# Kernel optimization log

Hardware: AMD Instinct MI355X
Metric: run time of the kernel (lower is better)

Reference implementation:

```python
import jax, jax.numpy as jnp
import numpy as np

D_MODEL = 256; N_HEADS = 8; N_LEVELS = 4; N_POINTS = 4; D_FFN = 1024
SHAPES = [(128, 128), (64, 64), (32, 32), (16, 16)]  # (H, W) per level, strides 8/16/32/64 of 1024x1024 input
B = 8; LQ = 1024
S_TOT = sum(h * w for h, w in SHAPES)


def setup_inputs() -> dict:
    key = jax.random.key(0)
    ks = iter(jax.random.split(key, 48))
    d = D_MODEL

    def f(shape, s=0.02):
        return jax.random.normal(next(ks), shape, dtype=jnp.float32) * s

    return {
        'tgt': f((B, LQ, d), 1.0),
        'query_pos': f((B, LQ, d), 1.0),
        'reference_points': jax.random.uniform(next(ks), (B, LQ, N_LEVELS, 2), dtype=jnp.float32),
        'src': f((B, S_TOT, d), 1.0),
        'w_in': f((3 * d, d)), 'b_in': jnp.zeros((3 * d,), jnp.float32),
        'w_out': f((d, d)), 'b_out': jnp.zeros((d,), jnp.float32),
        'ln1_g': jnp.ones((d,), jnp.float32), 'ln1_b': jnp.zeros((d,), jnp.float32),
        'ln2_g': jnp.ones((d,), jnp.float32), 'ln2_b': jnp.zeros((d,), jnp.float32),
        'ln3_g': jnp.ones((d,), jnp.float32), 'ln3_b': jnp.zeros((d,), jnp.float32),
        'w_val': f((d, d)), 'b_val': jnp.zeros((d,), jnp.float32),
        'w_off': f((N_HEADS * N_LEVELS * N_POINTS * 2, d), 0.002),
        'b_off': f((N_HEADS * N_LEVELS * N_POINTS * 2,), 0.5),
        'w_attw': f((N_HEADS * N_LEVELS * N_POINTS, d)),
        'b_attw': jnp.zeros((N_HEADS * N_LEVELS * N_POINTS,), jnp.float32),
        'w_oc': f((d, d)), 'b_oc': jnp.zeros((d,), jnp.float32),
        'w1': f((D_FFN, d)), 'b1': jnp.zeros((D_FFN,), jnp.float32),
        'w2': f((d, D_FFN)), 'b2': jnp.zeros((d,), jnp.float32),
        'spatial_shapes': jnp.array(SHAPES, dtype=jnp.int32),
    }


def layer_norm(x, g, b):
    mu = x.mean(-1, keepdims=True)
    var = ((x - mu) ** 2).mean(-1, keepdims=True)
    return (x - mu) * jax.lax.rsqrt(var + 1e-5) * g + b


def mha(tgt, query_pos, w_in, b_in, w_out, b_out):
    d = D_MODEL; Dh = d // N_HEADS
    Bs, Lq, _ = tgt.shape
    qk = tgt + query_pos
    q = (qk @ w_in[:d].T + b_in[:d]).reshape(Bs, Lq, N_HEADS, Dh)
    k = (qk @ w_in[d:2 * d].T + b_in[d:2 * d]).reshape(Bs, Lq, N_HEADS, Dh)
    v = (tgt @ w_in[2 * d:].T + b_in[2 * d:]).reshape(Bs, Lq, N_HEADS, Dh)
    attn = jax.nn.softmax(jnp.einsum('bqhd,bkhd->bhqk', q, k) / np.sqrt(Dh).astype(np.float32), axis=-1)
    o = jnp.einsum('bhqk,bkhd->bqhd', attn, v).reshape(Bs, Lq, d)
    return o @ w_out.T + b_out


def ms_deform_attn(value, loc, attw):
    # value [B,S,H,Dh]; loc [B,Lq,H,L,P,2] in [0,1]; attw [B,Lq,H,L,P]
    Bs, _, Hh, Dh = value.shape
    Lq = loc.shape[1]

    def to_hfirst(x):  # [B,Lq,Hh,P] -> [B,Hh,Lq*P,1]
        return jnp.transpose(x, (0, 2, 1, 3)).reshape(Bs, Hh, Lq * N_POINTS, 1)

    acc = jnp.zeros((Bs, Hh, Lq * N_POINTS, Dh), value.dtype)
    start = 0
    for l, (H_, W_) in enumerate(SHAPES):
        v = jnp.transpose(value[:, start:start + H_ * W_], (0, 2, 1, 3))  # [B,Hh,HW,Dh]
        start += H_ * W_
        ll = loc[:, :, :, l]  # [B,Lq,Hh,P,2]
        x = ll[..., 0] * W_ - 0.5
        y = ll[..., 1] * H_ - 0.5
        x0 = jnp.floor(x); y0 = jnp.floor(y)
        tx = x - x0; ty = y - y0

        def gather(xi, yi):
            valid = ((xi >= 0) & (xi < W_) & (yi >= 0) & (yi < H_)).astype(value.dtype)
            fi = (jnp.clip(yi, 0, H_ - 1) * W_ + jnp.clip(xi, 0, W_ - 1)).astype(jnp.int32)
            g = jnp.take_along_axis(v, to_hfirst(fi.astype(jnp.float32)).astype(jnp.int32), axis=2)
            return g * to_hfirst(valid)

        samp = (gather(x0, y0) * to_hfirst((1 - tx) * (1 - ty))
                + gather(x0 + 1, y0) * to_hfirst(tx * (1 - ty))
                + gather(x0, y0 + 1) * to_hfirst((1 - tx) * ty)
                + gather(x0 + 1, y0 + 1) * to_hfirst(tx * ty))
        acc = acc + samp * to_hfirst(attw[:, :, :, l])
    out = acc.reshape(Bs, Hh, Lq, N_POINTS, Dh).sum(3)  # [B,Hh,Lq,Dh]
    return jnp.transpose(out, (0, 2, 1, 3)).reshape(Bs, Lq, Hh * Dh)


def reference(tgt, query_pos, reference_points, src, w_in, b_in, w_out, b_out,
              ln1_g, ln1_b, ln2_g, ln2_b, ln3_g, ln3_b,
              w_val, b_val, w_off, b_off, w_attw, b_attw, w_oc, b_oc,
              w1, b1, w2, b2, spatial_shapes):
    Bs, Lq, d = tgt.shape
    Dh = d // N_HEADS
    # --- self attention (q=k=tgt+pos, v=tgt), residual + norm2 ---
    t2 = mha(tgt, query_pos, w_in, b_in, w_out, b_out)
    tgt = layer_norm(tgt + t2, ln2_g, ln2_b)
    # --- MSDeformAttn cross attention, residual + norm1 ---
    query = tgt + query_pos
    value = (src @ w_val.T + b_val).reshape(Bs, -1, N_HEADS, Dh)
    off = (query @ w_off.T + b_off).reshape(Bs, Lq, N_HEADS, N_LEVELS, N_POINTS, 2)
    aw = jax.nn.softmax((query @ w_attw.T + b_attw).reshape(Bs, Lq, N_HEADS, N_LEVELS * N_POINTS), axis=-1)
    aw = aw.reshape(Bs, Lq, N_HEADS, N_LEVELS, N_POINTS)
    normalizer = jnp.array([[w, h] for h, w in SHAPES], dtype=tgt.dtype)  # (W,H) per level
    loc = reference_points[:, :, None, :, None, :] + off / normalizer[None, None, None, :, None, :]
    ca = ms_deform_attn(value, loc, aw) @ w_oc.T + b_oc
    tgt = layer_norm(tgt + ca, ln1_g, ln1_b)
    # --- FFN, residual + norm3 ---
    t2 = jax.nn.relu(tgt @ w1.T + b1) @ w2.T + b2
    tgt = layer_norm(tgt + t2, ln3_g, ln3_b)
    return tgt
```

## Files before the change

kernel.cpp:

```cpp
#include <hip/hip_runtime.h>

typedef unsigned short ushort_t;
typedef unsigned int uint_t;
typedef __attribute__((ext_vector_type(8))) short short8;
typedef __attribute__((ext_vector_type(4))) float floatx4;
typedef __attribute__((ext_vector_type(4))) unsigned short ushortx4;

__device__ __forceinline__ ushort_t f2bf(float f){
  uint_t u = __builtin_bit_cast(uint_t, f);
  u += 0x7FFFu + ((u >> 16) & 1u);
  return (ushort_t)(u >> 16);
}
__device__ __forceinline__ float bf2f(ushort_t u){
  uint_t x = ((uint_t)u) << 16;
  return __builtin_bit_cast(float, x);
}
__device__ __forceinline__ uint_t packbf2(float a, float b){
  return (uint_t)f2bf(a) | ((uint_t)f2bf(b) << 16);
}

__device__ __forceinline__ void gload16(const void* g, void* l){
  __builtin_amdgcn_global_load_lds(
      (const __attribute__((address_space(1))) void*)g,
      (__attribute__((address_space(3))) void*)l, 16, 0, 0);
}

#define FENCED_BARRIER() asm volatile("s_barrier" ::: "memory")

__global__ __launch_bounds__(256) void convert_w_kernel(const float* __restrict__ w_in,
    const float* __restrict__ w_val, const float* __restrict__ w_out,
    const float* __restrict__ w_oc, const float* __restrict__ w1,
    const float* __restrict__ w2, const float* __restrict__ w_off,
    const float* __restrict__ w_attw, ushort_t* __restrict__ dst){
  int j = (blockIdx.x*256 + threadIdx.x) * 4;
  if (j >= 1015808) return;
  const float* src; int off;
  if      (j < 196608){ src = w_in;   off = 0;      }
  else if (j < 262144){ src = w_val;  off = 196608; }
  else if (j < 327680){ src = w_out;  off = 262144; }
  else if (j < 393216){ src = w_oc;   off = 327680; }
  else if (j < 655360){ src = w1;     off = 393216; }
  else if (j < 917504){ src = w2;     off = 655360; }
  else if (j < 983040){ src = w_off;  off = 917504; }
  else                { src = w_attw; off = 983040; }
  float4 v = *(const float4*)(src + (j - off));
  uint2 u; u.x = packbf2(v.x, v.y); u.y = packbf2(v.z, v.w);
  *(uint2*)(dst + j) = u;
}

__global__ __launch_bounds__(256) void pack_bias_kernel(const float* __restrict__ b_off,
    const float* __restrict__ b_attw, float* __restrict__ dst){
  int t = threadIdx.x;
  dst[t] = b_off[t];
  if (t < 128) dst[256 + t] = b_attw[t];
}

__global__ __launch_bounds__(256) void add_kernel(const float* __restrict__ a,
    const float* __restrict__ b, float* __restrict__ c, int n4){
  int i = blockIdx.x * 256 + threadIdx.x;
  if (i < n4){
    float4 x = ((const float4*)a)[i];
    float4 y = ((const float4*)b)[i];
    float4 z; z.x=x.x+y.x; z.y=x.y+y.y; z.z=x.z+y.z; z.w=x.w+y.w;
    ((float4*)c)[i] = z;
  }
}

__global__ __launch_bounds__(256) void addln_kernel(const float* __restrict__ X,
    const float* __restrict__ Y, const float* __restrict__ gw,
    const float* __restrict__ bw, float* __restrict__ Out){
  int wave = threadIdx.x >> 6, lane = threadIdx.x & 63;
  long row = (long)blockIdx.x * 4 + wave;
  long base = row * 256 + lane * 4;
  float4 x = *(const float4*)(X + base);
  float4 y = *(const float4*)(Y + base);
  float v0=x.x+y.x, v1=x.y+y.y, v2=x.z+y.z, v3=x.w+y.w;
  float s  = v0+v1+v2+v3;
  float sq = v0*v0+v1*v1+v2*v2+v3*v3;
  #pragma unroll
  for (int off=32; off>0; off>>=1){
    s  += __shfl_xor(s, off);
    sq += __shfl_xor(sq, off);
  }
  float mu  = s * (1.f/256.f);
  float var = sq * (1.f/256.f) - mu*mu;
  float rs  = rsqrtf(var + 1e-5f);
  float4 g4 = *(const float4*)(gw + lane*4);
  float4 b4 = *(const float4*)(bw + lane*4);
  float4 o;
  o.x = (v0-mu)*rs*g4.x + b4.x;
  o.y = (v1-mu)*rs*g4.y + b4.y;
  o.z = (v2-mu)*rs*g4.z + b4.z;
  o.w = (v3-mu)*rs*g4.w + b4.w;
  *(float4*)(Out + base) = o;
}

__device__ __forceinline__ void stage_copy16(ushort_t* ls, int r, int s, short8 v){
  int byte = r*64 + ((s ^ ((r>>1)&3)) << 4);
  *(short8*)((char*)ls + byte) = v;
}
__device__ __forceinline__ short8 frag_load(const ushort_t* ls, int r, int g){
  int byte = r*64 + ((g ^ ((r>>1)&3)) << 4);
  return *(const short8*)((const char*)ls + byte);
}

__device__ __forceinline__ short8 frag_load_f32(const float* ls, int r, int g){
  const char* base = (const char*)ls + r*128;
  int x = r & 7;
  float4 f0 = *(const float4*)(base + ((((2*g)  ^ x)) << 4));
  float4 f1 = *(const float4*)(base + ((((2*g+1)^ x)) << 4));
  uint4 u;
  u.x = packbf2(f0.x, f0.y); u.y = packbf2(f0.z, f0.w);
  u.z = packbf2(f1.x, f1.y); u.w = packbf2(f1.z, f1.w);
  return __builtin_bit_cast(short8, u);
}

template<bool RELU, bool OUT_BF16>
__global__ __launch_bounds__(256) void gemm_dma3_kernel(const float* __restrict__ A,
    const ushort_t* __restrict__ Wbf, const float* __restrict__ bias,
    void* __restrict__ Cout, int M, int N, int K){
  __shared__ float    ldsA[2][2048];
  __shared__ ushort_t ldsB[2][4096];
  const int t = threadIdx.x;
  const int lane = t & 63, wave = t >> 6;
  const int wm = wave >> 1, wn = wave & 1;
  const long rowA0 = (long)blockIdx.x * 64;
  const long rowB0 = (long)blockIdx.y * 128;
  const int rr = lane & 15, g = lane >> 4;
  const int arow_in = lane >> 3;
  const int aslot   = (lane & 7) ^ (arow_in & 7);
  const int brow_in = lane >> 2;
  const int bslot   = lane & 3;
  floatx4 acc[2][4] = {};
  const int nsteps = K >> 5;

  #define ISSUE3(kk, buf) do { \
    _Pragma("unroll") \
    for (int c=0;c<2;++c){ \
      int ar_ = wave*16 + c*8 + arow_in; \
      gload16(A + (rowA0 + ar_)*(long)K + (kk) + aslot*4, \
              &ldsA[buf][(wave*16 + c*8)*32]); \
    } \
    _Pragma("unroll") \
    for (int c=0;c<2;++c){ \
      int br_ = wave*32 + c*16 + brow_in; \
      const ushort_t* bs_ = Wbf + (rowB0 + br_)*(long)K + (kk) + (bslot ^ ((br_>>1)&3))*8; \
      gload16(bs_, (char*)ldsB[buf] + (wave*32 + c*16)*64); \
    } \
  } while(0)

  ISSUE3(0, 0);
  if (nsteps > 1) ISSUE3(32, 1);

  for (int k = 0; k < nsteps; ++k){
    if (k < nsteps-1) asm volatile("s_waitcnt vmcnt(4)" ::: "memory");
    else              asm volatile("s_waitcnt vmcnt(0)" ::: "memory");
    FENCED_BARRIER();
    const float*    lA = ldsA[k & 1];
    const ushort_t* lB = ldsB[k & 1];
    short8 af[2], bfr[4];
    #pragma unroll
    for (int mi=0;mi<2;++mi) af[mi]  = frag_load_f32(lA, wm*32 + mi*16 + rr, g);
    #pragma unroll
    for (int ni=0;ni<4;++ni) bfr[ni] = frag_load(lB, wn*64 + ni*16 + rr, g);
    #pragma unroll
    for (int mi=0;mi<2;++mi)
      #pragma unroll
      for (int ni=0;ni<4;++ni)
        acc[mi][ni] = __builtin_amdgcn_mfma_f32_16x16x32_bf16(af[mi], bfr[ni], acc[mi][ni], 0, 0, 0);
    FENCED_BARRIER();
    if (k + 2 < nsteps) ISSUE3((k+2)*32, k & 1);
  }
  #undef ISSUE3

  const int cg = lane >> 4;
  #pragma unroll
  for (int ni=0;ni<4;++ni){
    long n = rowB0 + wn*64 + ni*16 + (lane & 15);
    float bv = bias[n];
    #pragma unroll
    for (int mi=0;mi<2;++mi){
      long m = rowA0 + wm*32 + mi*16 + cg*4;
      #pragma unroll
      for (int r2=0;r2<4;++r2){
        float v = acc[mi][ni][r2] + bv;
        if (RELU) v = fmaxf(v, 0.f);
        if (OUT_BF16) ((ushort_t*)Cout)[(m+r2)*N + n] = f2bf(v);
        else          ((float*)Cout)[(m+r2)*N + n] = v;
      }
    }
  }
}

template<bool RELU, bool OUT_BF16>
__global__ __launch_bounds__(256) void gemm_dma5_kernel(const float* __restrict__ A,
    const ushort_t* __restrict__ Wbf, const float* __restrict__ bias,
    void* __restrict__ Cout, int M, int N, int K){
  __shared__ float    ldsA[2][2048];
  __shared__ ushort_t ldsB[2][8192];
  const int t = threadIdx.x;
  const int lane = t & 63, wave = t >> 6;
  const long rowA0 = (long)blockIdx.x * 64;
  const long rowB0 = (long)blockIdx.y * 256;
  const int rr = lane & 15, g = lane >> 4;
  const int arow_in = lane >> 3;
  const int aslot   = (lane & 7) ^ (arow_in & 7);
  const int brow_in = lane >> 2;
  const int bslot   = lane & 3;
  floatx4 acc[4][4] = {};
  const int nsteps = K >> 5;

  #define ISSUE5(kk, buf) do { \
    _Pragma("unroll") \
    for (int c=0;c<2;++c){ \
      int ar_ = wave*16 + c*8 + arow_in; \
      gload16(A + (rowA0 + ar_)*(long)K + (kk) + aslot*4, \
              &ldsA[buf][(wave*16 + c*8)*32]); \
    } \
    _Pragma("unroll") \
    for (int c=0;c<4;++c){ \
      int br_ = wave*64 + c*16 + brow_in; \
      const ushort_t* bs_ = Wbf + (rowB0 + br_)*(long)K + (kk) + (bslot ^ ((br_>>1)&3))*8; \
      gload16(bs_, (char*)ldsB[buf] + (wave*64 + c*16)*64); \
    } \
  } while(0)

  ISSUE5(0, 0);
  if (nsteps > 1) ISSUE5(32, 1);

  for (int k = 0; k < nsteps; ++k){
    if (k < nsteps-1) asm volatile("s_waitcnt vmcnt(6)" ::: "memory");
    else              asm volatile("s_waitcnt vmcnt(0)" ::: "memory");
    FENCED_BARRIER();
    const float*    lA = ldsA[k & 1];
    const ushort_t* lB = ldsB[k & 1];
    short8 af[4], bfr[4];
    #pragma unroll
    for (int mi=0;mi<4;++mi) af[mi]  = frag_load_f32(lA, mi*16 + rr, g);
    #pragma unroll
    for (int ni=0;ni<4;++ni) bfr[ni] = frag_load(lB, wave*64 + ni*16 + rr, g);
    #pragma unroll
    for (int mi=0;mi<4;++mi)
      #pragma unroll
      for (int ni=0;ni<4;++ni)
        acc[mi][ni] = __builtin_amdgcn_mfma_f32_16x16x32_bf16(bfr[ni], af[mi], acc[mi][ni], 0, 0, 0);
    FENCED_BARRIER();
    if (k + 2 < nsteps) ISSUE5((k+2)*32, k & 1);
  }
  #undef ISSUE5

  const int cg = lane >> 4;
  #pragma unroll
  for (int mi=0;mi<4;++mi){
    long m = rowA0 + mi*16 + (lane & 15);
    #pragma unroll
    for (int ni=0;ni<4;++ni){
      long n = rowB0 + wave*64 + ni*16 + cg*4;
      float4 bv = *(const float4*)(bias + n);
      float v0 = acc[mi][ni][0] + bv.x;
      float v1 = acc[mi][ni][1] + bv.y;
      float v2 = acc[mi][ni][2] + bv.z;
      float v3 = acc[mi][ni][3] + bv.w;
      if (RELU){ v0=fmaxf(v0,0.f); v1=fmaxf(v1,0.f); v2=fmaxf(v2,0.f); v3=fmaxf(v3,0.f); }
      if (OUT_BF16){
        uint2 pk; pk.x = packbf2(v0, v1); pk.y = packbf2(v2, v3);
        *(uint2*)((ushort_t*)Cout + m*(long)N + n) = pk;
      } else {
        float4 o; o.x=v0; o.y=v1; o.z=v2; o.w=v3;
        *(float4*)((float*)Cout + m*(long)N + n) = o;
      }
    }
  }
}

__global__ __launch_bounds__(256) void attn_mfma_kernel(const ushort_t* __restrict__ QK,
    const ushort_t* __restrict__ V, float* __restrict__ O){
  __shared__ ushort_t lsQ[4096];
  __shared__ ushort_t lsK[1024];
  __shared__ ushort_t lsVT[1024];
  __shared__ ushort_t lsP[4096];
  const int bh = blockIdx.y, b = bh >> 3, h = bh & 7;
  const int qt0 = blockIdx.x * 128;
  const int t = threadIdx.x, lane = t & 63, w = t >> 6;
  const int rr = lane & 15, g = lane >> 4;
  const float csc = 0.25506332f;

  const ushort_t* qbase = QK + ((long)b*1024 + qt0)*512 + h*32;
  #pragma unroll
  for (int j=0;j<2;++j){
    int i = t + j*256; int r = i>>2, s = i&3;
    short8 v = *(const short8*)(qbase + (long)r*512 + s*8);
    stage_copy16(lsQ, r, s, v);
  }
  __syncthreads();
  short8 bq[2];
  bq[0] = frag_load(lsQ, w*32 + rr, g);
  bq[1] = frag_load(lsQ, w*32 + 16 + rr, g);

  floatx4 accO[2][2] = {};
  float rsum[2] = {0.f, 0.f};
  const ushort_t* kbase = QK + (long)b*1024*512 + 256 + h*32;
  const ushort_t* vbase = V  + (long)b*1024*256 + h*32;

  for (int kt = 0; kt < 1024; kt += 32){
    __syncthreads();
    if (t < 128){
      int r = t >> 2, s = t & 3;
      short8 v = *(const short8*)(kbase + (long)(kt + r)*512 + s*8);
      stage_copy16(lsK, r, s, v);
    }
    {
      int kk = t >> 3, d4 = t & 7;
      ushortx4 vv = *(const ushortx4*)(vbase + (long)(kt + kk)*256 + d4*4);
      #pragma unroll
      for (int j=0;j<4;++j){
        int d = d4*4 + j;
        int cb = kk*2;
        int byte = d*64 + ((((cb>>4) ^ ((d>>1)&3)) << 4) | (cb & 15));
        *(ushort_t*)((char*)lsVT + byte) = vv[j];
      }
    }
    __syncthreads();
    floatx4 accS[2][2] = {};
    short8 ak0 = frag_load(lsK, rr, g);
    short8 ak1 = frag_load(lsK, 16 + rr, g);
    accS[0][0] = __builtin_amdgcn_mfma_f32_16x16x32_bf16(ak0, bq[0], accS[0][0], 0,0,0);
    accS[0][1] = __builtin_amdgcn_mfma_f32_16x16x32_bf16(ak0, bq[1], accS[0][1], 0,0,0);
    accS[1][0] = __builtin_amdgcn_mfma_f32_16x16x32_bf16(ak1, bq[0], accS[1][0], 0,0,0);
    accS[1][1] = __builtin_amdgcn_mfma_f32_16x16x32_bf16(ak1, bq[1], accS[1][1], 0,0,0);
    #pragma unroll
    for (int mi=0;mi<2;++mi){
      #pragma unroll
      for (int ni=0;ni<2;++ni){
        float p0 = exp2f(accS[mi][ni][0]*csc);
        float p1 = exp2f(accS[mi][ni][1]*csc);
        float p2 = exp2f(accS[mi][ni][2]*csc);
        float p3 = exp2f(accS[mi][ni][3]*csc);
        rsum[ni] += (p0+p1)+(p2+p3);
        int q   = w*32 + ni*16 + rr;
        int k0b = (mi*16 + g*4)*2;
        int byte = q*64 + ((((k0b>>4) ^ ((q>>1)&3)) << 4) | (k0b & 15));
        uint2 u; u.x = packbf2(p0,p1); u.y = packbf2(p2,p3);
        *(uint2*)((char*)lsP + byte) = u;
      }
    }
    short8 av0 = frag_load(lsVT, rr, g);
    short8 av1 = frag_load(lsVT, 16 + rr, g);
    short8 bp0 = frag_load(lsP, w*32 + rr, g);
    short8 bp1 = frag_load(lsP, w*32 + 16 + rr, g);
    accO[0][0] = __builtin_amdgcn_mfma_f32_16x16x32_bf16(av0, bp0, accO[0][0], 0,0,0);
    accO[0][1] = __builtin_amdgcn_mfma_f32_16x16x32_bf16(av0, bp1, accO[0][1], 0,0,0);
    accO[1][0] = __builtin_amdgcn_mfma_f32_16x16x32_bf16(av1, bp0, accO[1][0], 0,0,0);
    accO[1][1] = __builtin_amdgcn_mfma_f32_16x16x32_bf16(av1, bp1, accO[1][1], 0,0,0);
  }
  #pragma unroll
  for (int ni=0;ni<2;++ni){
    rsum[ni] += __shfl_xor(rsum[ni], 16);
    rsum[ni] += __shfl_xor(rsum[ni], 32);
    float inv = 1.f / rsum[ni];
    int q = qt0 + w*32 + ni*16 + rr;
    float* op = O + ((long)b*1024 + q)*256 + h*32;
    #pragma unroll
    for (int mi=0;mi<2;++mi){
      #pragma unroll
      for (int r2=0;r2<4;++r2){
        int d = mi*16 + g*4 + r2;
        op[d] = accO[mi][ni][r2] * inv;
      }
    }
  }
}

__global__ __launch_bounds__(256) void deform_kernel(const ushort_t* __restrict__ val,
    const float* __restrict__ offaw, const float* __restrict__ refp,
    float* __restrict__ Out){
  __shared__ float s_cat[1536], s_ref[32];
  const int t = threadIdx.x;
  const long q0 = (long)blockIdx.x * 4;
  const float* srcOA = offaw + q0*384;
  *(float4*)(s_cat + t*4) = *(const float4*)(srcOA + t*4);
  if (t < 128) *(float4*)(s_cat + 1024 + t*4) = *(const float4*)(srcOA + 1024 + t*4);
  if (t < 32)  s_ref[t] = refp[q0*8 + t];
  __syncthreads();
  const int qi = t >> 6, tl = t & 63;
  const int h = tl >> 3, dq = (tl & 7) << 2;
  const int bq = (int)q0 + qi;
  const int b = bq >> 10;
  const float* offp = s_cat + qi*384 + h*32;
  const float* awp  = s_cat + qi*384 + 256 + h*16;
  const float* refq = s_ref + qi*8;
  float mx = -1e30f;
  #pragma unroll
  for (int i=0;i<16;++i) mx = fmaxf(mx, awp[i]);
  float p[16], sum = 0.f;
  #pragma unroll
  for (int i=0;i<16;++i){ p[i] = expf(awp[i]-mx); sum += p[i]; }
  float inv = 1.f/sum;
  const long vb = (long)b*21760*256 + h*32 + dq;
  const int Dim[4] = {128,64,32,16};
  const int St[4]  = {0,16384,20480,21504};
  float a0=0.f, a1=0.f, a2=0.f, a3=0.f;
  #pragma unroll
  for (int l=0;l<4;++l){
    const int Wl = Dim[l], Hl = Dim[l], st = St[l];
    float rx = refq[2*l], ry = refq[2*l+1];
    #pragma unroll
    for (int pp=0;pp<4;++pp){
      float x = rx*(float)Wl + offp[l*8+pp*2]   - 0.5f;
      float y = ry*(float)Hl + offp[l*8+pp*2+1] - 0.5f;
      float xf = floorf(x), yf = floorf(y);
      int x0 = (int)xf, y0 = (int)yf;
      float tx = x - xf, ty = y - yf;
      float s0=0.f,s1=0.f,s2=0.f,s3=0.f;
      #define CORNER(XI, YI, WGT) { \
        int xi_ = (XI), yi_ = (YI); \
        bool valid_ = (xi_ >= 0) & (xi_ < Wl) & (yi_ >= 0) & (yi_ < Hl); \
        int xc_ = min(max(xi_, 0), Wl-1), yc_ = min(max(yi_, 0), Hl-1); \
        ushortx4 u = *(const ushortx4*)(val + vb + (long)(st + yc_*Wl + xc_)*256); \
        float wq = valid_ ? (WGT) : 0.f; \
        s0 += wq*bf2f(u[0]); s1 += wq*bf2f(u[1]); \
        s2 += wq*bf2f(u[2]); s3 += wq*bf2f(u[3]); \
      }
      CORNER(x0,   y0,   (1.f-tx)*(1.f-ty));
      CORNER(x0+1, y0,   tx*(1.f-ty));
      CORNER(x0,   y0+1, (1.f-tx)*ty);
      CORNER(x0+1, y0+1, tx*ty);
      #undef CORNER
      float pw = p[l*4+pp];
      a0 += pw*s0; a1 += pw*s1; a2 += pw*s2; a3 += pw*s3;
    }
  }
  float4 o; o.x=a0*inv; o.y=a1*inv; o.z=a2*inv; o.w=a3*inv;
  *(float4*)(Out + (long)bq*256 + h*32 + dq) = o;
}

extern "C" void kernel_launch(void* const* d_in, const int* in_sizes, int n_in,
                              void* d_out, int out_size, void* d_ws, size_t ws_size,
                              hipStream_t stream){
  (void)in_sizes; (void)n_in; (void)out_size; (void)ws_size;
  const float* tgt   = (const float*)d_in[0];
  const float* qpos  = (const float*)d_in[1];
  const float* refp  = (const float*)d_in[2];
  const float* src   = (const float*)d_in[3];
  const float* w_in  = (const float*)d_in[4];
  const float* b_in  = (const float*)d_in[5];
  const float* w_out = (const float*)d_in[6];
  const float* b_out = (const float*)d_in[7];
  const float* ln1g  = (const float*)d_in[8];
  const float* ln1b  = (const float*)d_in[9];
  const float* ln2g  = (const float*)d_in[10];
  const float* ln2b  = (const float*)d_in[11];
  const float* ln3g  = (const float*)d_in[12];
  const float* ln3b  = (const float*)d_in[13];
  const float* w_val = (const float*)d_in[14];
  const float* b_val = (const float*)d_in[15];
  const float* w_off = (const float*)d_in[16];
  const float* b_off = (const float*)d_in[17];
  const float* w_attw= (const float*)d_in[18];
  const float* b_attw= (const float*)d_in[19];
  const float* w_oc  = (const float*)d_in[20];
  const float* b_oc  = (const float*)d_in[21];
  const float* w1    = (const float*)d_in[22];
  const float* b1    = (const float*)d_in[23];
  const float* w2    = (const float*)d_in[24];
  const float* b2    = (const float*)d_in[25];

  float* ws = (float*)d_ws;
  ushort_t* bufWbf = (ushort_t*)ws;
  float* bufBOA = ws + 507904;
  float* bufQ   = ws + 524288;
  float* bufOA  = ws + 524288;
  ushort_t* bufQK = (ushort_t*)(ws + 2621440);
  ushort_t* bufV  = (ushort_t*)(ws + 4718592);
  float* bufO   = ws + 5767168;
  float* bufT2  = ws + 7864320;
  float* bufTg1 = ws + 9961472;
  float* bufTg2 = ws + 12058624;
  ushort_t* bufVal = (ushort_t*)(ws + 16777216);
  float* bufH   = ws + 16777216;
  float* outF   = (float*)d_out;

  const ushort_t* winbf    = bufWbf;
  const ushort_t* winvbf   = bufWbf + 131072;
  const ushort_t* wvalbf   = bufWbf + 196608;
  const ushort_t* woutbf   = bufWbf + 262144;
  const ushort_t* wocbf    = bufWbf + 327680;
  const ushort_t* w1bf     = bufWbf + 393216;
  const ushort_t* w2bf     = bufWbf + 655360;
  const ushort_t* woffawbf = bufWbf + 917504;

  dim3 B256(256);
  convert_w_kernel<<<dim3(992), B256, 0, stream>>>(w_in, w_val, w_out, w_oc, w1, w2, w_off, w_attw, bufWbf);
  pack_bias_kernel<<<dim3(1), B256, 0, stream>>>(b_off, b_attw, bufBOA);
  add_kernel<<<dim3(2048), B256, 0, stream>>>(tgt, qpos, bufQ, 524288);
  gemm_dma3_kernel<false,true><<<dim3(128,4), B256, 0, stream>>>(bufQ, winbf, b_in, bufQK, 8192, 512, 256);
  gemm_dma3_kernel<false,true><<<dim3(128,2), B256, 0, stream>>>(tgt, winvbf, b_in + 512, bufV, 8192, 256, 256);
  attn_mfma_kernel<<<dim3(8,64), B256, 0, stream>>>(bufQK, bufV, bufO);
  gemm_dma3_kernel<false,false><<<dim3(128,2), B256, 0, stream>>>(bufO, woutbf, b_out, bufT2, 8192, 256, 256);
  addln_kernel<<<dim3(2048), B256, 0, stream>>>(tgt, bufT2, ln2g, ln2b, bufTg1);
  gemm_dma5_kernel<false,true><<<dim3(2720,1), B256, 0, stream>>>(src, wvalbf, b_val, bufVal, 174080, 256, 256);
  add_kernel<<<dim3(2048), B256, 0, stream>>>(bufTg1, qpos, bufT2, 524288);
  gemm_dma3_kernel<false,false><<<dim3(128,3), B256, 0, stream>>>(bufT2, woffawbf, bufBOA, bufOA, 8192, 384, 256);
  deform_kernel<<<dim3(2048), B256, 0, stream>>>(bufVal, bufOA, refp, bufO);
  gemm_dma3_kernel<false,false><<<dim3(128,2), B256, 0, stream>>>(bufO, wocbf, b_oc, bufT2, 8192, 256, 256);
  addln_kernel<<<dim3(2048), B256, 0, stream>>>(bufTg1, bufT2, ln1g, ln1b, bufTg2);
  gemm_dma5_kernel<true,false><<<dim3(128,4), B256, 0, stream>>>(bufTg2, w1bf, b1, bufH, 8192, 1024, 256);
  gemm_dma3_kernel<false,false><<<dim3(128,2), B256, 0, stream>>>(bufH, w2bf, b2, bufT2, 8192, 256, 1024);
  addln_kernel<<<dim3(2048), B256, 0, stream>>>(bufTg2, bufT2, ln3g, ln3b, outF);
}
```

Measured before the change: 305.1 us.

## Add register-resident weight GEMM for K=256 and use it for most projections

Adds a GEMM kernel that keeps each wave's full 64x256 bf16 weight slice in registers and streams A rows straight from global memory, with no LDS staging and no barriers. It replaces the LDS double-buffered dma3/dma5 kernels for the QK, V, out-proj, value-proj (16-row groups, 4 per block), output-conv and FFN1 GEMMs. This removes LDS traffic and synchronisation. In exchange, weights are reloaded per block, register pressure rises (128 VGPRs for weights) and A loads are uncoalesced-ish direct loads.

```diff
diff --git a/kernel.cpp b/kernel.cpp
--- a/kernel.cpp
+++ b/kernel.cpp
@@ -115,6 +115,83 @@
   return __builtin_bit_cast(short8, u);
 }
 
+__device__ __forceinline__ short8 pack_frag(float4 f0, float4 f1){
+  uint4 u;
+  u.x = packbf2(f0.x, f0.y); u.y = packbf2(f0.z, f0.w);
+  u.z = packbf2(f1.x, f1.y); u.w = packbf2(f1.z, f1.w);
+  return __builtin_bit_cast(short8, u);
+}
+
+template<int G, bool RELU, bool OUT_BF16>
+__global__ __launch_bounds__(256) void gemm_wreg_kernel(const float* __restrict__ A,
+    const ushort_t* __restrict__ Wbf, const float* __restrict__ bias,
+    void* __restrict__ Cout, int M, int N){
+  const int t = threadIdx.x, lane = t & 63, wave = t >> 6;
+  const int rr = lane & 15, g = lane >> 4;
+  const long n0 = (long)blockIdx.y * 256 + wave * 64;
+  const long m0 = (long)blockIdx.x * (16*G);
+
+  short8 bw[4][8];
+  #pragma unroll
+  for (int nt=0;nt<4;++nt)
+    #pragma unroll
+    for (int ks=0;ks<8;++ks)
+      bw[nt][ks] = *(const short8*)(Wbf + (n0 + nt*16 + rr)*256 + ks*32 + g*8);
+
+  float4 bias4[4];
+  #pragma unroll
+  for (int nt=0;nt<4;++nt) bias4[nt] = *(const float4*)(bias + n0 + nt*16 + g*4);
+
+  for (int si=0; si<G; ++si){
+    const long m = m0 + si*16;
+    const float* Ap = A + (m + rr)*256 + g*8;
+    float4 f[8];
+    #pragma unroll
+    for (int ks=0;ks<4;++ks){
+      f[2*ks]   = *(const float4*)(Ap + ks*32);
+      f[2*ks+1] = *(const float4*)(Ap + ks*32 + 4);
+    }
+    short8 av[4];
+    #pragma unroll
+    for (int ks=0;ks<4;++ks) av[ks] = pack_frag(f[2*ks], f[2*ks+1]);
+    #pragma unroll
+    for (int ks=0;ks<4;++ks){
+      f[2*ks]   = *(const float4*)(Ap + 128 + ks*32);
+      f[2*ks+1] = *(const float4*)(Ap + 128 + ks*32 + 4);
+    }
+    floatx4 acc[4] = {};
+    #pragma unroll
+    for (int ks=0;ks<4;++ks)
+      #pragma unroll
+      for (int nt=0;nt<4;++nt)
+        acc[nt] = __builtin_amdgcn_mfma_f32_16x16x32_bf16(bw[nt][ks], av[ks], acc[nt], 0, 0, 0);
+    #pragma unroll
+    for (int ks=0;ks<4;++ks) av[ks] = pack_frag(f[2*ks], f[2*ks+1]);
+    #pragma unroll
+    for (int ks=0;ks<4;++ks)
+      #pragma unroll
+      for (int nt=0;nt<4;++nt)
+        acc[nt] = __builtin_amdgcn_mfma_f32_16x16x32_bf16(bw[nt][ks+4], av[ks], acc[nt], 0, 0, 0);
+    const long mrow = m + rr;
+    #pragma unroll
+    for (int nt=0;nt<4;++nt){
+      long n = n0 + nt*16 + g*4;
+      float v0 = acc[nt][0] + bias4[nt].x;
+      float v1 = acc[nt][1] + bias4[nt].y;
+      float v2 = acc[nt][2] + bias4[nt].z;
+      float v3 = acc[nt][3] + bias4[nt].w;
+      if (RELU){ v0=fmaxf(v0,0.f); v1=fmaxf(v1,0.f); v2=fmaxf(v2,0.f); v3=fmaxf(v3,0.f); }
+      if (OUT_BF16){
+        uint2 pk; pk.x = packbf2(v0, v1); pk.y = packbf2(v2, v3);
+        *(uint2*)((ushort_t*)Cout + mrow*(long)N + n) = pk;
+      } else {
+        float4 o; o.x=v0; o.y=v1; o.z=v2; o.w=v3;
+        *(float4*)((float*)Cout + mrow*(long)N + n) = o;
+      }
+    }
+  }
+}
+
 template<bool RELU, bool OUT_BF16>
 __global__ __launch_bounds__(256) void gemm_dma3_kernel(const float* __restrict__ A,
     const ushort_t* __restrict__ Wbf, const float* __restrict__ bias,
@@ -187,87 +264,6 @@
         if (RELU) v = fmaxf(v, 0.f);
         if (OUT_BF16) ((ushort_t*)Cout)[(m+r2)*N + n] = f2bf(v);
         else          ((float*)Cout)[(m+r2)*N + n] = v;
-      }
-    }
-  }
-}
-
-template<bool RELU, bool OUT_BF16>
-__global__ __launch_bounds__(256) void gemm_dma5_kernel(const float* __restrict__ A,
-    const ushort_t* __restrict__ Wbf, const float* __restrict__ bias,
-    void* __restrict__ Cout, int M, int N, int K){
-  __shared__ float    ldsA[2][2048];
-  __shared__ ushort_t ldsB[2][8192];
-  const int t = threadIdx.x;
-  const int lane = t & 63, wave = t >> 6;
-  const long rowA0 = (long)blockIdx.x * 64;
-  const long rowB0 = (long)blockIdx.y * 256;
-  const int rr = lane & 15, g = lane >> 4;
-  const int arow_in = lane >> 3;
-  const int aslot   = (lane & 7) ^ (arow_in & 7);
-  const int brow_in = lane >> 2;
-  const int bslot   = lane & 3;
-  floatx4 acc[4][4] = {};
-  const int nsteps = K >> 5;
-
-  #define ISSUE5(kk, buf) do { \
-    _Pragma("unroll") \
-    for (int c=0;c<2;++c){ \
-      int ar_ = wave*16 + c*8 + arow_in; \
-      gload16(A + (rowA0 + ar_)*(long)K + (kk) + aslot*4, \
-              &ldsA[buf][(wave*16 + c*8)*32]); \
-    } \
-    _Pragma("unroll") \
-    for (int c=0;c<4;++c){ \
-      int br_ = wave*64 + c*16 + brow_in; \
-      const ushort_t* bs_ = Wbf + (rowB0 + br_)*(long)K + (kk) + (bslot ^ ((br_>>1)&3))*8; \
-      gload16(bs_, (char*)ldsB[buf] + (wave*64 + c*16)*64); \
-    } \
-  } while(0)
-
-  ISSUE5(0, 0);
-  if (nsteps > 1) ISSUE5(32, 1);
-
-  for (int k = 0; k < nsteps; ++k){
-    if (k < nsteps-1) asm volatile("s_waitcnt vmcnt(6)" ::: "memory");
-    else              asm volatile("s_waitcnt vmcnt(0)" ::: "memory");
-    FENCED_BARRIER();
-    const float*    lA = ldsA[k & 1];
-    const ushort_t* lB = ldsB[k & 1];
-    short8 af[4], bfr[4];
-    #pragma unroll
-    for (int mi=0;mi<4;++mi) af[mi]  = frag_load_f32(lA, mi*16 + rr, g);
-    #pragma unroll
-    for (int ni=0;ni<4;++ni) bfr[ni] = frag_load(lB, wave*64 + ni*16 + rr, g);
-    #pragma unroll
-    for (int mi=0;mi<4;++mi)
-      #pragma unroll
-      for (int ni=0;ni<4;++ni)
-        acc[mi][ni] = __builtin_amdgcn_mfma_f32_16x16x32_bf16(bfr[ni], af[mi], acc[mi][ni], 0, 0, 0);
-    FENCED_BARRIER();
-    if (k + 2 < nsteps) ISSUE5((k+2)*32, k & 1);
-  }
-  #undef ISSUE5
-
-  const int cg = lane >> 4;
-  #pragma unroll
-  for (int mi=0;mi<4;++mi){
-    long m = rowA0 + mi*16 + (lane & 15);
-    #pragma unroll
-    for (int ni=0;ni<4;++ni){
-      long n = rowB0 + wave*64 + ni*16 + cg*4;
-      float4 bv = *(const float4*)(bias + n);
-      float v0 = acc[mi][ni][0] + bv.x;
-      float v1 = acc[mi][ni][1] + bv.y;
-      float v2 = acc[mi][ni][2] + bv.z;
-      float v3 = acc[mi][ni][3] + bv.w;
-      if (RELU){ v0=fmaxf(v0,0.f); v1=fmaxf(v1,0.f); v2=fmaxf(v2,0.f); v3=fmaxf(v3,0.f); }
-      if (OUT_BF16){
-        uint2 pk; pk.x = packbf2(v0, v1); pk.y = packbf2(v2, v3);
-        *(uint2*)((ushort_t*)Cout + m*(long)N + n) = pk;
-      } else {
-        float4 o; o.x=v0; o.y=v1; o.z=v2; o.w=v3;
-        *(float4*)((float*)Cout + m*(long)N + n) = o;
       }
     }
   }
@@ -493,18 +489,18 @@
   convert_w_kernel<<<dim3(992), B256, 0, stream>>>(w_in, w_val, w_out, w_oc, w1, w2, w_off, w_attw, bufWbf);
   pack_bias_kernel<<<dim3(1), B256, 0, stream>>>(b_off, b_attw, bufBOA);
   add_kernel<<<dim3(2048), B256, 0, stream>>>(tgt, qpos, bufQ, 524288);
-  gemm_dma3_kernel<false,true><<<dim3(128,4), B256, 0, stream>>>(bufQ, winbf, b_in, bufQK, 8192, 512, 256);
-  gemm_dma3_kernel<false,true><<<dim3(128,2), B256, 0, stream>>>(tgt, winvbf, b_in + 512, bufV, 8192, 256, 256);
+  gemm_wreg_kernel<1,false,true><<<dim3(512,2), B256, 0, stream>>>(bufQ, winbf, b_in, bufQK, 8192, 512);
+  gemm_wreg_kernel<1,false,true><<<dim3(512,1), B256, 0, stream>>>(tgt, winvbf, b_in + 512, bufV, 8192, 256);
   attn_mfma_kernel<<<dim3(8,64), B256, 0, stream>>>(bufQK, bufV, bufO);
-  gemm_dma3_kernel<false,false><<<dim3(128,2), B256, 0, stream>>>(bufO, woutbf, b_out, bufT2, 8192, 256, 256);
+  gemm_wreg_kernel<1,false,false><<<dim3(512,1), B256, 0, stream>>>(bufO, woutbf, b_out, bufT2, 8192, 256);
   addln_kernel<<<dim3(2048), B256, 0, stream>>>(tgt, bufT2, ln2g, ln2b, bufTg1);
-  gemm_dma5_kernel<false,true><<<dim3(2720,1), B256, 0, stream>>>(src, wvalbf, b_val, bufVal, 174080, 256, 256);
+  gemm_wreg_kernel<4,false,true><<<dim3(2720,1), B256, 0, stream>>>(src, wvalbf, b_val, bufVal, 174080, 256);
   add_kernel<<<dim3(2048), B256, 0, stream>>>(bufTg1, qpos, bufT2, 524288);
   gemm_dma3_kernel<false,false><<<dim3(128,3), B256, 0, stream>>>(bufT2, woffawbf, bufBOA, bufOA, 8192, 384, 256);
   deform_kernel<<<dim3(2048), B256, 0, stream>>>(bufVal, bufOA, refp, bufO);
-  gemm_dma3_kernel<false,false><<<dim3(128,2), B256, 0, stream>>>(bufO, wocbf, b_oc, bufT2, 8192, 256, 256);
+  gemm_wreg_kernel<1,false,false><<<dim3(512,1), B256, 0, stream>>>(bufO, wocbf, b_oc, bufT2, 8192, 256);
   addln_kernel<<<dim3(2048), B256, 0, stream>>>(bufTg1, bufT2, ln1g, ln1b, bufTg2);
-  gemm_dma5_kernel<true,false><<<dim3(128,4), B256, 0, stream>>>(bufTg2, w1bf, b1, bufH, 8192, 1024, 256);
+  gemm_wreg_kernel<1,true,false><<<dim3(512,4), B256, 0, stream>>>(bufTg2, w1bf, b1, bufH, 8192, 1024);
   gemm_dma3_kernel<false,false><<<dim3(128,2), B256, 0, stream>>>(bufH, w2bf, b2, bufT2, 8192, 256, 1024);
   addln_kernel<<<dim3(2048), B256, 0, stream>>>(bufTg2, bufT2, ln3g, ln3b, outF);
 }
```

Result: slower. 475.6 us (+55.9%).
